# Kernel tuning notes

Measured on AMD Instinct MI355X. Metric: run time of the kernel, lower is better.

Reference implementation:

```python
import jax, jax.numpy as jnp
import numpy as np


def setup_inputs() -> dict:
    key = jax.random.key(0)
    ks = jax.random.split(key, 8)
    B, W, H, C = 4, 64, 64, 256
    C2 = C // 2
    s = 0.05
    x = jax.random.normal(ks[0], (B, W, H, C), dtype=jnp.float32)
    Wq = jax.random.normal(ks[1], (C, C2), dtype=jnp.float32) * s
    bq = jax.random.normal(ks[2], (C2,), dtype=jnp.float32) * s
    Wk = jax.random.normal(ks[3], (C, C2), dtype=jnp.float32) * s
    bk = jax.random.normal(ks[4], (C2,), dtype=jnp.float32) * s
    Wv = jax.random.normal(ks[5], (C, C), dtype=jnp.float32) * s
    bv = jax.random.normal(ks[6], (C,), dtype=jnp.float32) * s
    # gamma is initialized to 0 in the original; use a nonzero value so the
    # attention branch actually contributes (math is identical).
    gamma = jnp.array([0.5], dtype=jnp.float32)
    return {"x": x, "Wq": Wq, "bq": bq, "Wk": Wk, "bk": bk, "Wv": Wv, "bv": bv, "gamma": gamma}


def reference(x, Wq, bq, Wk, bk, Wv, bv, gamma):
    B, W, H, C = x.shape
    N = W * H
    # 1x1 convs == per-pixel linear projections
    q = jnp.einsum('bwhc,cd->bwhd', x, Wq) + bq   # [B,W,H,C/2]
    k = jnp.einsum('bwhc,cd->bwhd', x, Wk) + bk   # [B,W,H,C/2]
    v = jnp.einsum('bwhc,cd->bwhd', x, Wv) + bv   # [B,W,H,C]
    # Faithful to original: raw row-major reshape (B,W,H,Cq) -> (B,Cq,N)
    # (this mixes spatial and channel axes, exactly as the TF code does)
    pq = q.reshape(B, -1, N)                      # [B,C/2,N]
    pk = k.reshape(B, -1, N)                      # [B,C/2,N]
    pv = v.reshape(B, -1, N)                      # [B,C,N]
    energy = jnp.einsum('bcn,bcm->bnm', pq, pk)   # [B,N,N] (pq transposed)
    attention = jax.nn.softmax(energy, axis=-1)   # [B,N,N]
    out = jnp.einsum('bcm,bnm->bcn', pv, attention)  # pv @ attention^T
    out = out.reshape(B, W, H, C)
    return gamma * out + x
```

## Files before the change

kernel.cpp:

```cpp
#include <hip/hip_runtime.h>
#include <hip/hip_bf16.h>
#include <stdint.h>


typedef __attribute__((ext_vector_type(8)))  short short8;
typedef __attribute__((ext_vector_type(4)))  float f32x4;
typedef __attribute__((ext_vector_type(16))) float f32x16;
typedef __attribute__((ext_vector_type(4)))  unsigned short u16x4;

#define MFMA16 __builtin_amdgcn_mfma_f32_16x16x32_bf16
#define MFMA32 __builtin_amdgcn_mfma_f32_32x32x16_bf16

__device__ __forceinline__ unsigned short f2bf(float f) {
    union { float f; uint32_t u; } v; v.f = f;
    return (unsigned short)((v.u + 0x8000u) >> 16);
}
__device__ __forceinline__ float bf2f(unsigned short h) {
    union { uint32_t u; float f; } v; v.u = ((uint32_t)h) << 16;
    return v.f;
}
__device__ __forceinline__ uint32_t pkbf(float a, float b) {
    union { __hip_bfloat162 h; uint32_t u; } v;
    v.h = __float22bfloat162_rn(float2{a, b});
    return v.u;
}

__global__ void prep_w(const float* __restrict__ Wq, const float* __restrict__ bq,
                       const float* __restrict__ Wk, const float* __restrict__ bk,
                       const float* __restrict__ Wv, const float* __restrict__ bv,
                       unsigned short* __restrict__ Wt, float* __restrict__ bias) {
    int g = blockIdx.x * 256 + threadIdx.x;
    int c = g & 255, d = g >> 8;
    float val;
    if (d < 128)      val = Wq[c * 128 + d];
    else if (d < 256) val = Wk[c * 128 + (d - 128)];
    else              val = Wv[c * 256 + (d - 256)];
    Wt[d * 256 + c] = f2bf(val);
    if (g < 512) {
        float bb;
        if (g < 128)      bb = bq[g];
        else if (g < 256) bb = bk[g - 128];
        else              bb = bv[g - 256];
        bias[g] = bb;
    }
}

__global__ __launch_bounds__(256) void proj(
        const float* __restrict__ x, const unsigned short* __restrict__ Wt,
        const float* __restrict__ bias,
        unsigned short* __restrict__ Qrm, unsigned short* __restrict__ Kp,
        unsigned short* __restrict__ Vp) {
    __shared__ unsigned short T[128 * 136];
    int bid = blockIdx.x;
    int tid = threadIdx.x;
    int wave = tid >> 6, lane = tid & 63;
    int l16 = lane & 15, quad = lane >> 4;

    int kind, b, a, vh = 0;
    if (bid < 256) { kind = bid >> 7; int s = bid & 127; b = s >> 5; a = s & 31; }
    else           { kind = 2; int s = bid - 256; vh = s >> 7; b = (s >> 5) & 3; a = s & 31; }

    short8 af[2][8];
    #pragma unroll
    for (int g = 0; g < 2; ++g) {
        int p_local = wave * 32 + g * 16 + l16;
        int pix = (kind == 2) ? (b * 4096 + a * 128 + p_local)
                              : (b * 4096 + a + 32 * p_local);
        const float* xr = x + (size_t)pix * 256;
        #pragma unroll
        for (int kk = 0; kk < 8; ++kk) {
            f32x4 u0 = *(const f32x4*)(xr + kk * 32 + quad * 8);
            f32x4 u1 = *(const f32x4*)(xr + kk * 32 + quad * 8 + 4);
            union { short8 s; uint32_t u[4]; } h;
            h.u[0] = pkbf(u0[0], u0[1]); h.u[1] = pkbf(u0[2], u0[3]);
            h.u[2] = pkbf(u1[0], u1[1]); h.u[3] = pkbf(u1[2], u1[3]);
            af[g][kk] = h.s;
        }
    }

    if (kind < 2) {
        int dbase = kind * 128;
        #pragma unroll 1
        for (int dt = 0; dt < 8; ++dt) {
            int d = dbase + dt * 16 + l16;
            float bval = bias[d];
            f32x4 acc0 = {0.f,0.f,0.f,0.f}, acc1 = {0.f,0.f,0.f,0.f};
            #pragma unroll
            for (int kk = 0; kk < 8; ++kk) {
                short8 wrow = *(const short8*)(Wt + d * 256 + kk * 32 + quad * 8);
                acc0 = MFMA16(af[0][kk], wrow, acc0, 0, 0, 0);
                acc1 = MFMA16(af[1][kk], wrow, acc1, 0, 0, 0);
            }
            #pragma unroll
            for (int g = 0; g < 2; ++g) {
                f32x4 acc = g ? acc1 : acc0;
                union { u16x4 v; uint32_t u[2]; } pk;
                pk.u[0] = pkbf(acc[0] + bval, acc[1] + bval);
                pk.u[1] = pkbf(acc[2] + bval, acc[3] + bval);
                *(u16x4*)(T + (dt * 16 + l16) * 136 + wave * 32 + g * 16 + quad * 4) = pk.v;
            }
        }
        __syncthreads();
        if (kind == 0) {
            unsigned short* ob = Qrm + (b << 19) + a * 128 * 128;
            #pragma unroll
            for (int it = 0; it < 8; ++it) {
                int ci = it * 256 + tid;
                int row = ci >> 4, cj = ci & 15;
                *(short8*)(ob + row * 128 + cj * 8) = *(const short8*)(T + row * 136 + cj * 8);
            }
        } else {
            unsigned short* kb = Kp + (b << 19);
            #pragma unroll
            for (int it = 0; it < 8; ++it) {
                int ci = it * 256 + tid;
                int row = ci >> 4, cj = ci & 15;
                *(short8*)(kb + (cj >> 1) * 65536 + (a * 128 + row) * 16 + (cj & 1) * 8)
                    = *(const short8*)(T + row * 136 + cj * 8);
            }
        }
    } else {
        #pragma unroll 1
        for (int dt = 0; dt < 8; ++dt) {
            int d = 256 + vh * 128 + dt * 16 + l16;
            f32x4 acc0 = {0.f,0.f,0.f,0.f}, acc1 = {0.f,0.f,0.f,0.f};
            #pragma unroll
            for (int kk = 0; kk < 8; ++kk) {
                short8 wrow = *(const short8*)(Wt + d * 256 + kk * 32 + quad * 8);
                acc0 = MFMA16(wrow, af[0][kk], acc0, 0, 0, 0);
                acc1 = MFMA16(wrow, af[1][kk], acc1, 0, 0, 0);
            }
            int dvl = dt * 16 + quad * 4;
            f32x4 bv4 = *(const f32x4*)(bias + 256 + vh * 128 + dvl);
            #pragma unroll
            for (int g = 0; g < 2; ++g) {
                f32x4 acc = g ? acc1 : acc0;
                union { u16x4 v; uint32_t u[2]; } pk;
                pk.u[0] = pkbf(acc[0] + bv4[0], acc[1] + bv4[1]);
                pk.u[1] = pkbf(acc[2] + bv4[2], acc[3] + bv4[3]);
                int p_local = wave * 32 + g * 16 + l16;
                *(u16x4*)(T + p_local * 136 + dvl) = pk.v;
            }
        }
        __syncthreads();
        unsigned short* vb = Vp + (b << 20);
        #pragma unroll
        for (int it = 0; it < 8; ++it) {
            int cid = it * 256 + tid;
            int c_local = cid >> 8, w = cid & 255;
            int p_local = c_local * 16 + (w >> 4);
            int chunk = (w >> 4) * 16 + vh * 8 + ((w & 15) >> 1);
            *(short8*)(vb + chunk * 4096 + (a * 8 + c_local) * 16 + (w & 1) * 8)
                = *(const short8*)(T + p_local * 136 + (w & 15) * 8);
        }
    }
}

__global__ __launch_bounds__(256, 2) void attn(
        const unsigned short* __restrict__ Qrm, const unsigned short* __restrict__ Kp,
        const unsigned short* __restrict__ Vp, unsigned short* __restrict__ Opart,
        float* __restrict__ Lpart) {
    __shared__ unsigned short Ps[2 * 64 * 72];

    int bid = blockIdx.x;
    int comb = bid & 7, qt = bid >> 3;
    int b = comb >> 1, ks = comb & 1;
    int tid = threadIdx.x, wave = tid >> 6, lane = tid & 63;
    int l32 = lane & 31, half = lane >> 5;
    int mt = wave & 1, nt = wave >> 1;

    const unsigned short* Qb = Qrm + (b << 19);
    const unsigned short* Kb = Kp + (b << 19);
    const unsigned short* Vb = Vp + (b << 20);

    int q0 = qt * 64;

    short8 qf[8];
    {
        const unsigned short* qrow = Qb + (q0 + nt * 32 + l32) * 128 + half * 8;
        #pragma unroll
        for (int kk = 0; kk < 8; ++kk) qf[kk] = *(const short8*)(qrow + kk * 16);
    }

    f32x16 O[2][2];
    #pragma unroll
    for (int i = 0; i < 2; ++i)
        #pragma unroll
        for (int j = 0; j < 2; ++j)
            #pragma unroll
            for (int r = 0; r < 16; ++r) O[i][j][r] = 0.f;
    float l_run = 0.f;

    const int m_base = ks * 2048;
    const int chunk_base = ks * 128;

    int krow = (m_base + mt * 32 + l32) * 16 + half * 8;
    short8 kf[8];
    #pragma unroll
    for (int kk = 0; kk < 8; ++kk)
        kf[kk] = *(const short8*)(Kb + kk * 65536 + krow);
    short8 vfrag[2][4];
    #pragma unroll
    for (int c2 = 0; c2 < 2; ++c2)
        #pragma unroll
        for (int k2 = 0; k2 < 4; ++k2)
            vfrag[c2][k2] = *(const short8*)(Vb + (chunk_base + k2) * 4096
                              + ((wave * 2 + c2) * 32 + l32) * 16 + half * 8);

    #pragma unroll 1
    for (int kt = 0; kt < 32; ++kt) {
        unsigned short* Pb = Ps + (kt & 1) * (64 * 72);

        f32x16 S;
        #pragma unroll
        for (int r = 0; r < 16; ++r) S[r] = 0.f;
        #pragma unroll
        for (int kk = 0; kk < 8; ++kk) S = MFMA32(kf[kk], qf[kk], S, 0, 0, 0);

        #pragma unroll
        for (int g = 0; g < 4; ++g) {
            float p0 = __expf(S[g * 4 + 0]), p1 = __expf(S[g * 4 + 1]);
            float p2 = __expf(S[g * 4 + 2]), p3 = __expf(S[g * 4 + 3]);
            l_run += (p0 + p1) + (p2 + p3);
            union { u16x4 v; uint32_t u[2]; } pk;
            pk.u[0] = pkbf(p0, p1); pk.u[1] = pkbf(p2, p3);
            *(u16x4*)(Pb + (nt * 32 + l32) * 72 + mt * 32 + g * 8 + half * 4) = pk.v;
        }

        __syncthreads();

        if (kt < 31) {
            int kr1 = (m_base + (kt + 1) * 64 + mt * 32 + l32) * 16 + half * 8;
            #pragma unroll
            for (int kk = 0; kk < 8; ++kk)
                kf[kk] = *(const short8*)(Kb + kk * 65536 + kr1);
        }

        #pragma unroll
        for (int k2 = 0; k2 < 4; ++k2) {
            short8 pa0 = *(const short8*)(Pb + (l32) * 72 + k2 * 16 + half * 8);
            short8 pa1 = *(const short8*)(Pb + (32 + l32) * 72 + k2 * 16 + half * 8);
            O[0][0] = MFMA32(pa0, vfrag[0][k2], O[0][0], 0, 0, 0);
            O[0][1] = MFMA32(pa0, vfrag[1][k2], O[0][1], 0, 0, 0);
            O[1][0] = MFMA32(pa1, vfrag[0][k2], O[1][0], 0, 0, 0);
            O[1][1] = MFMA32(pa1, vfrag[1][k2], O[1][1], 0, 0, 0);
        }

        if (kt < 31) {
            int ch1 = chunk_base + (kt + 1) * 4;
            #pragma unroll
            for (int c2 = 0; c2 < 2; ++c2)
                #pragma unroll
                for (int k2 = 0; k2 < 4; ++k2)
                    vfrag[c2][k2] = *(const short8*)(Vb + (ch1 + k2) * 4096
                                      + ((wave * 2 + c2) * 32 + l32) * 16 + half * 8);
        }
    }

    l_run += __shfl_xor(l_run, 32);
    unsigned short* Op = Opart + ((size_t)(ks * 4 + b) << 20);
    #pragma unroll
    for (int q2 = 0; q2 < 2; ++q2)
        #pragma unroll
        for (int c2 = 0; c2 < 2; ++c2) {
            int c = (wave * 2 + c2) * 32 + l32;
            #pragma unroll
            for (int r = 0; r < 16; ++r) {
                int n = q0 + q2 * 32 + (r & 3) + 8 * (r >> 2) + 4 * half;
                Op[(size_t)n * 256 + c] = f2bf(O[q2][c2][r]);
            }
        }
    if (half == 0) {
        int n = q0 + nt * 32 + l32;
        Lpart[((ks * 2 + mt) * 4 + b) * 4096 + n] = l_run;
    }
}

__global__ __launch_bounds__(256) void merge_out(
        const unsigned short* __restrict__ Opart, const float* __restrict__ Lpart,
        const float* __restrict__ x, const float* __restrict__ gamma,
        float* __restrict__ out) {
    __shared__ float tile[64 * 257];
    __shared__ float wsm[64];
    int b  = blockIdx.x >> 6;
    int n0 = (blockIdx.x & 63) << 6;
    int tid = threadIdx.x;
    float g = gamma[0];
    if (tid < 64) {
        int n = n0 + tid;
        float L = 0.f;
        #pragma unroll
        for (int s = 0; s < 4; ++s) L += Lpart[(s * 4 + b) * 4096 + n];
        wsm[tid] = g / L;
    }
    __syncthreads();
    int nl1 = tid >> 5, cb1 = (tid & 31) * 8;
    const unsigned short* Op0 = Opart + ((size_t)(0 * 4 + b) << 20);
    const unsigned short* Op1 = Opart + ((size_t)(1 * 4 + b) << 20);
    #pragma unroll
    for (int i = 0; i < 8; ++i) {
        int nl = i * 8 + nl1;
        size_t off = (size_t)(n0 + nl) * 256 + cb1;
        short8 o0 = *(const short8*)(Op0 + off);
        short8 o1 = *(const short8*)(Op1 + off);
        float w = wsm[nl];
        float* tr = tile + nl * 257 + cb1;
        #pragma unroll
        for (int e = 0; e < 8; ++e)
            tr[e] = (bf2f((unsigned short)o0[e]) + bf2f((unsigned short)o1[e])) * w;
    }
    __syncthreads();
    int cg = tid >> 4, nq = (tid & 15) * 4;
    #pragma unroll
    for (int it = 0; it < 16; ++it) {
        int c = it * 16 + cg;
        size_t idx = ((size_t)b << 20) + (size_t)c * 4096 + n0 + nq;
        f32x4 xv = *(const f32x4*)(x + idx);
        f32x4 ov;
        #pragma unroll
        for (int e = 0; e < 4; ++e) ov[e] = tile[(nq + e) * 257 + c] + xv[e];
        *(f32x4*)(out + idx) = ov;
    }
}

extern "C" void kernel_launch(void* const* d_in, const int* in_sizes, int n_in,
                              void* d_out, int out_size, void* d_ws, size_t ws_size,
                              hipStream_t stream) {
    const float* x     = (const float*)d_in[0];
    const float* Wq    = (const float*)d_in[1];
    const float* bq    = (const float*)d_in[2];
    const float* Wk    = (const float*)d_in[3];
    const float* bk    = (const float*)d_in[4];
    const float* Wv    = (const float*)d_in[5];
    const float* bv    = (const float*)d_in[6];
    const float* gamma = (const float*)d_in[7];
    float* out = (float*)d_out;

    if (ws_size < 34080768u) return;

    char* ws = (char*)d_ws;
    unsigned short* Wt    = (unsigned short*)(ws);
    float*          bias  = (float*)        (ws +   262144);
    unsigned short* Qrm   = (unsigned short*)(ws +   264192);
    unsigned short* Kp    = (unsigned short*)(ws +  4458496);
    unsigned short* Vp    = (unsigned short*)(ws +  8652800);
    unsigned short* Opart = (unsigned short*)(ws + 17041408);
    float*          Lpart = (float*)        (ws + 33818624);

    prep_w   <<<512, 256, 0, stream>>>(Wq, bq, Wk, bk, Wv, bv, Wt, bias);
    proj     <<<512, 256, 0, stream>>>(x, Wt, bias, Qrm, Kp, Vp);
    attn     <<<512, 256, 0, stream>>>(Qrm, Kp, Vp, Opart, Lpart);
    merge_out<<<256, 256, 0, stream>>>(Opart, Lpart, x, gamma, out);
}
```

Measured before the change: 175.4 us.

## Fuse merge into attention kernel and drop key-split partials

Restructures the attention kernel so each block handles 32 query rows over the full key range instead of 64 rows over half the keys. Softmax normalization, gamma scaling and the residual add now happen in the attention epilogue via shared memory, which removes the bf16 partial-output buffers and the separate merge kernel. The goal is to cut global traffic for the partials and one kernel launch. In exchange, each block does half the query rows, so K and V fragments are loaded twice as often per query, and more vfrag registers may lower occupancy.

```diff
diff --git a/kernel.cpp b/kernel.cpp
--- a/kernel.cpp
+++ b/kernel.cpp
@@ -14,10 +14,6 @@
 __device__ __forceinline__ unsigned short f2bf(float f) {
     union { float f; uint32_t u; } v; v.f = f;
     return (unsigned short)((v.u + 0x8000u) >> 16);
-}
-__device__ __forceinline__ float bf2f(unsigned short h) {
-    union { uint32_t u; float f; } v; v.u = ((uint32_t)h) << 16;
-    return v.f;
 }
 __device__ __forceinline__ uint32_t pkbf(float a, float b) {
     union { __hip_bfloat162 h; uint32_t u; } v;
@@ -158,58 +154,58 @@
 
 __global__ __launch_bounds__(256, 2) void attn(
         const unsigned short* __restrict__ Qrm, const unsigned short* __restrict__ Kp,
-        const unsigned short* __restrict__ Vp, unsigned short* __restrict__ Opart,
-        float* __restrict__ Lpart) {
-    __shared__ unsigned short Ps[2 * 64 * 72];
+        const unsigned short* __restrict__ Vp, const float* __restrict__ x,
+        const float* __restrict__ gamma, float* __restrict__ out) {
+    __shared__ __align__(16) char smem[256 * 36 * 4];
+    __shared__ float Ls[4][32];
+    __shared__ float lwv[32];
+    unsigned short* Ps = (unsigned short*)smem;
+    float* Os = (float*)smem;
 
     int bid = blockIdx.x;
-    int comb = bid & 7, qt = bid >> 3;
-    int b = comb >> 1, ks = comb & 1;
+    int b = bid & 3, qt = bid >> 2;
     int tid = threadIdx.x, wave = tid >> 6, lane = tid & 63;
     int l32 = lane & 31, half = lane >> 5;
-    int mt = wave & 1, nt = wave >> 1;
 
     const unsigned short* Qb = Qrm + (b << 19);
     const unsigned short* Kb = Kp + (b << 19);
     const unsigned short* Vb = Vp + (b << 20);
 
-    int q0 = qt * 64;
+    int n0 = qt * 32;
+    float gm = gamma[0];
 
     short8 qf[8];
     {
-        const unsigned short* qrow = Qb + (q0 + nt * 32 + l32) * 128 + half * 8;
+        const unsigned short* qrow = Qb + (n0 + l32) * 128 + half * 8;
         #pragma unroll
         for (int kk = 0; kk < 8; ++kk) qf[kk] = *(const short8*)(qrow + kk * 16);
     }
 
-    f32x16 O[2][2];
-    #pragma unroll
-    for (int i = 0; i < 2; ++i)
-        #pragma unroll
-        for (int j = 0; j < 2; ++j)
-            #pragma unroll
-            for (int r = 0; r < 16; ++r) O[i][j][r] = 0.f;
+    f32x16 O[2];
+    #pragma unroll
+    for (int j = 0; j < 2; ++j)
+        #pragma unroll
+        for (int r = 0; r < 16; ++r) O[j][r] = 0.f;
     float l_run = 0.f;
 
-    const int m_base = ks * 2048;
-    const int chunk_base = ks * 128;
-
-    int krow = (m_base + mt * 32 + l32) * 16 + half * 8;
     short8 kf[8];
-    #pragma unroll
-    for (int kk = 0; kk < 8; ++kk)
-        kf[kk] = *(const short8*)(Kb + kk * 65536 + krow);
-    short8 vfrag[2][4];
+    {
+        int m0 = (wave * 32 + l32) * 16 + half * 8;
+        #pragma unroll
+        for (int kk = 0; kk < 8; ++kk)
+            kf[kk] = *(const short8*)(Kb + kk * 65536 + m0);
+    }
+    short8 vfrag[2][8];
     #pragma unroll
     for (int c2 = 0; c2 < 2; ++c2)
         #pragma unroll
-        for (int k2 = 0; k2 < 4; ++k2)
-            vfrag[c2][k2] = *(const short8*)(Vb + (chunk_base + k2) * 4096
+        for (int k2 = 0; k2 < 8; ++k2)
+            vfrag[c2][k2] = *(const short8*)(Vb + k2 * 4096
                               + ((wave * 2 + c2) * 32 + l32) * 16 + half * 8);
 
     #pragma unroll 1
     for (int kt = 0; kt < 32; ++kt) {
-        unsigned short* Pb = Ps + (kt & 1) * (64 * 72);
+        unsigned short* Pb = Ps + (kt & 1) * (32 * 136);
 
         f32x16 S;
         #pragma unroll
@@ -224,102 +220,68 @@
             l_run += (p0 + p1) + (p2 + p3);
             union { u16x4 v; uint32_t u[2]; } pk;
             pk.u[0] = pkbf(p0, p1); pk.u[1] = pkbf(p2, p3);
-            *(u16x4*)(Pb + (nt * 32 + l32) * 72 + mt * 32 + g * 8 + half * 4) = pk.v;
+            *(u16x4*)(Pb + l32 * 136 + wave * 32 + g * 8 + half * 4) = pk.v;
         }
 
         __syncthreads();
 
         if (kt < 31) {
-            int kr1 = (m_base + (kt + 1) * 64 + mt * 32 + l32) * 16 + half * 8;
+            int m1 = ((kt + 1) * 128 + wave * 32 + l32) * 16 + half * 8;
             #pragma unroll
             for (int kk = 0; kk < 8; ++kk)
-                kf[kk] = *(const short8*)(Kb + kk * 65536 + kr1);
-        }
-
-        #pragma unroll
-        for (int k2 = 0; k2 < 4; ++k2) {
-            short8 pa0 = *(const short8*)(Pb + (l32) * 72 + k2 * 16 + half * 8);
-            short8 pa1 = *(const short8*)(Pb + (32 + l32) * 72 + k2 * 16 + half * 8);
-            O[0][0] = MFMA32(pa0, vfrag[0][k2], O[0][0], 0, 0, 0);
-            O[0][1] = MFMA32(pa0, vfrag[1][k2], O[0][1], 0, 0, 0);
-            O[1][0] = MFMA32(pa1, vfrag[0][k2], O[1][0], 0, 0, 0);
-            O[1][1] = MFMA32(pa1, vfrag[1][k2], O[1][1], 0, 0, 0);
+                kf[kk] = *(const short8*)(Kb + kk * 65536 + m1);
+        }
+
+        #pragma unroll
+        for (int k2 = 0; k2 < 8; ++k2) {
+            short8 pa = *(const short8*)(Pb + l32 * 136 + k2 * 16 + half * 8);
+            O[0] = MFMA32(pa, vfrag[0][k2], O[0], 0, 0, 0);
+            O[1] = MFMA32(pa, vfrag[1][k2], O[1], 0, 0, 0);
         }
 
         if (kt < 31) {
-            int ch1 = chunk_base + (kt + 1) * 4;
+            int ch1 = (kt + 1) * 8;
             #pragma unroll
             for (int c2 = 0; c2 < 2; ++c2)
                 #pragma unroll
-                for (int k2 = 0; k2 < 4; ++k2)
+                for (int k2 = 0; k2 < 8; ++k2)
                     vfrag[c2][k2] = *(const short8*)(Vb + (ch1 + k2) * 4096
                                       + ((wave * 2 + c2) * 32 + l32) * 16 + half * 8);
         }
     }
 
     l_run += __shfl_xor(l_run, 32);
-    unsigned short* Op = Opart + ((size_t)(ks * 4 + b) << 20);
-    #pragma unroll
-    for (int q2 = 0; q2 < 2; ++q2)
-        #pragma unroll
-        for (int c2 = 0; c2 < 2; ++c2) {
-            int c = (wave * 2 + c2) * 32 + l32;
-            #pragma unroll
-            for (int r = 0; r < 16; ++r) {
-                int n = q0 + q2 * 32 + (r & 3) + 8 * (r >> 2) + 4 * half;
-                Op[(size_t)n * 256 + c] = f2bf(O[q2][c2][r]);
-            }
-        }
-    if (half == 0) {
-        int n = q0 + nt * 32 + l32;
-        Lpart[((ks * 2 + mt) * 4 + b) * 4096 + n] = l_run;
-    }
-}
-
-__global__ __launch_bounds__(256) void merge_out(
-        const unsigned short* __restrict__ Opart, const float* __restrict__ Lpart,
-        const float* __restrict__ x, const float* __restrict__ gamma,
-        float* __restrict__ out) {
-    __shared__ float tile[64 * 257];
-    __shared__ float wsm[64];
-    int b  = blockIdx.x >> 6;
-    int n0 = (blockIdx.x & 63) << 6;
-    int tid = threadIdx.x;
-    float g = gamma[0];
-    if (tid < 64) {
-        int n = n0 + tid;
-        float L = 0.f;
-        #pragma unroll
-        for (int s = 0; s < 4; ++s) L += Lpart[(s * 4 + b) * 4096 + n];
-        wsm[tid] = g / L;
-    }
+    if (half == 0) Ls[wave][l32] = l_run;
     __syncthreads();
-    int nl1 = tid >> 5, cb1 = (tid & 31) * 8;
-    const unsigned short* Op0 = Opart + ((size_t)(0 * 4 + b) << 20);
-    const unsigned short* Op1 = Opart + ((size_t)(1 * 4 + b) << 20);
-    #pragma unroll
-    for (int i = 0; i < 8; ++i) {
-        int nl = i * 8 + nl1;
-        size_t off = (size_t)(n0 + nl) * 256 + cb1;
-        short8 o0 = *(const short8*)(Op0 + off);
-        short8 o1 = *(const short8*)(Op1 + off);
-        float w = wsm[nl];
-        float* tr = tile + nl * 257 + cb1;
-        #pragma unroll
-        for (int e = 0; e < 8; ++e)
-            tr[e] = (bf2f((unsigned short)o0[e]) + bf2f((unsigned short)o1[e])) * w;
-    }
+    if (tid < 32)
+        lwv[tid] = gm / (Ls[0][tid] + Ls[1][tid] + Ls[2][tid] + Ls[3][tid]);
     __syncthreads();
-    int cg = tid >> 4, nq = (tid & 15) * 4;
-    #pragma unroll
-    for (int it = 0; it < 16; ++it) {
-        int c = it * 16 + cg;
-        size_t idx = ((size_t)b << 20) + (size_t)c * 4096 + n0 + nq;
+
+    #pragma unroll
+    for (int c2 = 0; c2 < 2; ++c2) {
+        int c = (wave * 2 + c2) * 32 + l32;
+        #pragma unroll
+        for (int g = 0; g < 4; ++g) {
+            f32x4 gv = *(const f32x4*)(lwv + g * 8 + half * 4);
+            f32x4 ov;
+            #pragma unroll
+            for (int i = 0; i < 4; ++i) ov[i] = O[c2][g * 4 + i] * gv[i];
+            *(f32x4*)(Os + c * 36 + g * 8 + half * 4) = ov;
+        }
+    }
+    __syncthreads();
+
+    int n4 = tid & 7, cg = tid >> 3;
+    #pragma unroll
+    for (int it = 0; it < 8; ++it) {
+        int c = it * 32 + cg;
+        f32x4 ov = *(const f32x4*)(Os + c * 36 + n4 * 4);
+        size_t idx = ((size_t)b << 20) + (size_t)c * 4096 + n0 + n4 * 4;
         f32x4 xv = *(const f32x4*)(x + idx);
-        f32x4 ov;
-        #pragma unroll
-        for (int e = 0; e < 4; ++e) ov[e] = tile[(nq + e) * 257 + c] + xv[e];
-        *(f32x4*)(out + idx) = ov;
+        f32x4 rv;
+        #pragma unroll
+        for (int e = 0; e < 4; ++e) rv[e] = ov[e] + xv[e];
+        *(f32x4*)(out + idx) = rv;
     }
 }
 
@@ -336,7 +298,7 @@
     const float* gamma = (const float*)d_in[7];
     float* out = (float*)d_out;
 
-    if (ws_size < 34080768u) return;
+    if (ws_size < 17041408u) return;
 
     char* ws = (char*)d_ws;
     unsigned short* Wt    = (unsigned short*)(ws);
@@ -344,11 +306,8 @@
     unsigned short* Qrm   = (unsigned short*)(ws +   264192);
     unsigned short* Kp    = (unsigned short*)(ws +  4458496);
     unsigned short* Vp    = (unsigned short*)(ws +  8652800);
-    unsigned short* Opart = (unsigned short*)(ws + 17041408);
-    float*          Lpart = (float*)        (ws + 33818624);
-
-    prep_w   <<<512, 256, 0, stream>>>(Wq, bq, Wk, bk, Wv, bv, Wt, bias);
-    proj     <<<512, 256, 0, stream>>>(x, Wt, bias, Qrm, Kp, Vp);
-    attn     <<<512, 256, 0, stream>>>(Qrm, Kp, Vp, Opart, Lpart);
-    merge_out<<<256, 256, 0, stream>>>(Opart, Lpart, x, gamma, out);
-}
+
+    prep_w<<<512, 256, 0, stream>>>(Wq, bq, Wk, bk, Wv, bv, Wt, bias);
+    proj  <<<512, 256, 0, stream>>>(x, Wt, bias, Qrm, Kp, Vp);
+    attn  <<<512, 256, 0, stream>>>(Qrm, Kp, Vp, x, gamma, out);
+}
```

Result: slower. 180.8 us (+3.1%).

## Fuse all four phases into one cooperative kernel with grid-wide syncs

Applied to the files above, without the earlier changes.

Turns the prep, projection, attention and merge kernels into device phases and runs them inside a single cooperative kernel of 512 blocks, separated by grid.sync(), with shared memory reused across phases. The merge phase is re-tiled to 32 rows per block so it also uses 512 blocks. This aims to remove the launch gaps and tail idle time between the four launches. In exchange it adds grid-barrier cost, forces one launch-bounds and shared-memory size on all phases, and falls back to separate launches if the cooperative launch fails.

```diff
diff --git a/kernel.cpp b/kernel.cpp
--- a/kernel.cpp
+++ b/kernel.cpp
@@ -1,6 +1,9 @@
 #include <hip/hip_runtime.h>
 #include <hip/hip_bf16.h>
+#include <hip/hip_cooperative_groups.h>
 #include <stdint.h>
+
+namespace cg = cooperative_groups;
 
 
 typedef __attribute__((ext_vector_type(8)))  short short8;
@@ -11,6 +14,8 @@
 #define MFMA16 __builtin_amdgcn_mfma_f32_16x16x32_bf16
 #define MFMA32 __builtin_amdgcn_mfma_f32_32x32x16_bf16
 
+#define SMEM_BYTES 34816
+
 __device__ __forceinline__ unsigned short f2bf(float f) {
     union { float f; uint32_t u; } v; v.f = f;
     return (unsigned short)((v.u + 0x8000u) >> 16);
@@ -25,11 +30,13 @@
     return v.u;
 }
 
-__global__ void prep_w(const float* __restrict__ Wq, const float* __restrict__ bq,
-                       const float* __restrict__ Wk, const float* __restrict__ bk,
-                       const float* __restrict__ Wv, const float* __restrict__ bv,
-                       unsigned short* __restrict__ Wt, float* __restrict__ bias) {
-    int g = blockIdx.x * 256 + threadIdx.x;
+__device__ __forceinline__ void phase_prep(
+        int bid, int tid,
+        const float* __restrict__ Wq, const float* __restrict__ bq,
+        const float* __restrict__ Wk, const float* __restrict__ bk,
+        const float* __restrict__ Wv, const float* __restrict__ bv,
+        unsigned short* __restrict__ Wt, float* __restrict__ bias) {
+    int g = bid * 256 + tid;
     int c = g & 255, d = g >> 8;
     float val;
     if (d < 128)      val = Wq[c * 128 + d];
@@ -45,14 +52,13 @@
     }
 }
 
-__global__ __launch_bounds__(256) void proj(
+__device__ __forceinline__ void phase_proj(
+        char* smem, int bid, int tid,
         const float* __restrict__ x, const unsigned short* __restrict__ Wt,
         const float* __restrict__ bias,
         unsigned short* __restrict__ Qrm, unsigned short* __restrict__ Kp,
         unsigned short* __restrict__ Vp) {
-    __shared__ unsigned short T[128 * 136];
-    int bid = blockIdx.x;
-    int tid = threadIdx.x;
+    unsigned short* T = (unsigned short*)smem;
     int wave = tid >> 6, lane = tid & 63;
     int l16 = lane & 15, quad = lane >> 4;
 
@@ -156,16 +162,16 @@
     }
 }
 
-__global__ __launch_bounds__(256, 2) void attn(
+__device__ __forceinline__ void phase_attn(
+        char* smem, int bid, int tid,
         const unsigned short* __restrict__ Qrm, const unsigned short* __restrict__ Kp,
         const unsigned short* __restrict__ Vp, unsigned short* __restrict__ Opart,
         float* __restrict__ Lpart) {
-    __shared__ unsigned short Ps[2 * 64 * 72];
-
-    int bid = blockIdx.x;
+    unsigned short* Ps = (unsigned short*)smem;
+
     int comb = bid & 7, qt = bid >> 3;
     int b = comb >> 1, ks = comb & 1;
-    int tid = threadIdx.x, wave = tid >> 6, lane = tid & 63;
+    int wave = tid >> 6, lane = tid & 63;
     int l32 = lane & 31, half = lane >> 5;
     int mt = wave & 1, nt = wave >> 1;
 
@@ -204,7 +210,7 @@
     for (int c2 = 0; c2 < 2; ++c2)
         #pragma unroll
         for (int k2 = 0; k2 < 4; ++k2)
-            vfrag[c2][k2] = *(const short8*)(Vb + (chunk_base + k2) * 4096
+            vfrag[c2][k2] = *(const short8*)(Vp + (b << 20) + (chunk_base + k2) * 4096
                               + ((wave * 2 + c2) * 32 + l32) * 16 + half * 8);
 
     #pragma unroll 1
@@ -276,17 +282,17 @@
     }
 }
 
-__global__ __launch_bounds__(256) void merge_out(
+__device__ __forceinline__ void phase_merge(
+        char* smem, int bid, int tid,
         const unsigned short* __restrict__ Opart, const float* __restrict__ Lpart,
         const float* __restrict__ x, const float* __restrict__ gamma,
         float* __restrict__ out) {
-    __shared__ float tile[64 * 257];
-    __shared__ float wsm[64];
-    int b  = blockIdx.x >> 6;
-    int n0 = (blockIdx.x & 63) << 6;
-    int tid = threadIdx.x;
+    float* tile = (float*)smem;
+    float* wsm  = (float*)smem + 32 * 257;
+    int b  = bid >> 7;
+    int n0 = (bid & 127) << 5;
     float g = gamma[0];
-    if (tid < 64) {
+    if (tid < 32) {
         int n = n0 + tid;
         float L = 0.f;
         #pragma unroll
@@ -295,10 +301,10 @@
     }
     __syncthreads();
     int nl1 = tid >> 5, cb1 = (tid & 31) * 8;
-    const unsigned short* Op0 = Opart + ((size_t)(0 * 4 + b) << 20);
-    const unsigned short* Op1 = Opart + ((size_t)(1 * 4 + b) << 20);
-    #pragma unroll
-    for (int i = 0; i < 8; ++i) {
+    const unsigned short* Op0 = Opart + ((size_t)b << 20);
+    const unsigned short* Op1 = Opart + ((size_t)(4 + b) << 20);
+    #pragma unroll
+    for (int i = 0; i < 4; ++i) {
         int nl = i * 8 + nl1;
         size_t off = (size_t)(n0 + nl) * 256 + cb1;
         short8 o0 = *(const short8*)(Op0 + off);
@@ -310,10 +316,10 @@
             tr[e] = (bf2f((unsigned short)o0[e]) + bf2f((unsigned short)o1[e])) * w;
     }
     __syncthreads();
-    int cg = tid >> 4, nq = (tid & 15) * 4;
-    #pragma unroll
-    for (int it = 0; it < 16; ++it) {
-        int c = it * 16 + cg;
+    int cg2 = tid >> 3, nq = (tid & 7) * 4;
+    #pragma unroll
+    for (int it = 0; it < 8; ++it) {
+        int c = it * 32 + cg2;
         size_t idx = ((size_t)b << 20) + (size_t)c * 4096 + n0 + nq;
         f32x4 xv = *(const f32x4*)(x + idx);
         f32x4 ov;
@@ -321,6 +327,49 @@
         for (int e = 0; e < 4; ++e) ov[e] = tile[(nq + e) * 257 + c] + xv[e];
         *(f32x4*)(out + idx) = ov;
     }
+}
+
+__global__ void __launch_bounds__(256, 2) fused_all(
+        const float* x, const float* Wq, const float* bq, const float* Wk,
+        const float* bk, const float* Wv, const float* bv, const float* gamma,
+        float* out, unsigned short* Wt, float* bias, unsigned short* Qrm,
+        unsigned short* Kp, unsigned short* Vp, unsigned short* Opart,
+        float* Lpart) {
+    __shared__ __align__(16) char smem[SMEM_BYTES];
+    cg::grid_group grid = cg::this_grid();
+    int bid = blockIdx.x, tid = threadIdx.x;
+
+    phase_prep(bid, tid, Wq, bq, Wk, bk, Wv, bv, Wt, bias);
+    grid.sync();
+    phase_proj(smem, bid, tid, x, Wt, bias, Qrm, Kp, Vp);
+    grid.sync();
+    phase_attn(smem, bid, tid, Qrm, Kp, Vp, Opart, Lpart);
+    grid.sync();
+    phase_merge(smem, bid, tid, Opart, Lpart, x, gamma, out);
+}
+
+__global__ void prep_w_k(const float* Wq, const float* bq, const float* Wk,
+                         const float* bk, const float* Wv, const float* bv,
+                         unsigned short* Wt, float* bias) {
+    phase_prep(blockIdx.x, threadIdx.x, Wq, bq, Wk, bk, Wv, bv, Wt, bias);
+}
+__global__ __launch_bounds__(256) void proj_k(
+        const float* x, const unsigned short* Wt, const float* bias,
+        unsigned short* Qrm, unsigned short* Kp, unsigned short* Vp) {
+    __shared__ __align__(16) char smem[SMEM_BYTES];
+    phase_proj(smem, blockIdx.x, threadIdx.x, x, Wt, bias, Qrm, Kp, Vp);
+}
+__global__ __launch_bounds__(256, 2) void attn_k(
+        const unsigned short* Qrm, const unsigned short* Kp,
+        const unsigned short* Vp, unsigned short* Opart, float* Lpart) {
+    __shared__ __align__(16) char smem[18432];
+    phase_attn(smem, blockIdx.x, threadIdx.x, Qrm, Kp, Vp, Opart, Lpart);
+}
+__global__ __launch_bounds__(256) void merge_k(
+        const unsigned short* Opart, const float* Lpart, const float* x,
+        const float* gamma, float* out) {
+    __shared__ __align__(16) char smem[33024];
+    phase_merge(smem, blockIdx.x, threadIdx.x, Opart, Lpart, x, gamma, out);
 }
 
 extern "C" void kernel_launch(void* const* d_in, const int* in_sizes, int n_in,
@@ -347,8 +396,17 @@
     unsigned short* Opart = (unsigned short*)(ws + 17041408);
     float*          Lpart = (float*)        (ws + 33818624);
 
-    prep_w   <<<512, 256, 0, stream>>>(Wq, bq, Wk, bk, Wv, bv, Wt, bias);
-    proj     <<<512, 256, 0, stream>>>(x, Wt, bias, Qrm, Kp, Vp);
-    attn     <<<512, 256, 0, stream>>>(Qrm, Kp, Vp, Opart, Lpart);
-    merge_out<<<256, 256, 0, stream>>>(Opart, Lpart, x, gamma, out);
-}
+    void* args[] = { (void*)&x, (void*)&Wq, (void*)&bq, (void*)&Wk, (void*)&bk,
+                     (void*)&Wv, (void*)&bv, (void*)&gamma, (void*)&out,
+                     (void*)&Wt, (void*)&bias, (void*)&Qrm, (void*)&Kp,
+                     (void*)&Vp, (void*)&Opart, (void*)&Lpart };
+    hipError_t err = hipLaunchCooperativeKernel((const void*)fused_all,
+                                                dim3(512), dim3(256),
+                                                args, 0, stream);
+    if (err != hipSuccess) {
+        prep_w_k<<<512, 256, 0, stream>>>(Wq, bq, Wk, bk, Wv, bv, Wt, bias);
+        proj_k  <<<512, 256, 0, stream>>>(x, Wt, bias, Qrm, Kp, Vp);
+        attn_k  <<<512, 256, 0, stream>>>(Qrm, Kp, Vp, Opart, Lpart);
+        merge_k <<<512, 256, 0, stream>>>(Opart, Lpart, x, gamma, out);
+    }
+}
```

Measured after the change: 365.9 us. +108.6%, slower.

## Software-pipeline QK^T and softmax one tile ahead of PV in attention loop

Applied to the files above, without the earlier changes.

Restructures the main attention loop so the S=K·Q MFMA, exp, and P store for tile kt+1 run before the PV MFMAs of tile kt. K fragments are prefetched two tiles ahead. This lets the exp/VALU work overlap with the matrix-core work across the barrier and hides K load latency better. The cost is higher register pressure from holding extra prefetched K fragments, plus a prologue that duplicates the first tile's work.

```diff
diff --git a/kernel.cpp b/kernel.cpp
--- a/kernel.cpp
+++ b/kernel.cpp
@@ -193,12 +193,12 @@
 
     const int m_base = ks * 2048;
     const int chunk_base = ks * 128;
-
-    int krow = (m_base + mt * 32 + l32) * 16 + half * 8;
+    const int kbase = (m_base + mt * 32 + l32) * 16 + half * 8;
+
     short8 kf[8];
     #pragma unroll
     for (int kk = 0; kk < 8; ++kk)
-        kf[kk] = *(const short8*)(Kb + kk * 65536 + krow);
+        kf[kk] = *(const short8*)(Kb + kk * 65536 + kbase);
     short8 vfrag[2][4];
     #pragma unroll
     for (int c2 = 0; c2 < 2; ++c2)
@@ -206,17 +206,12 @@
         for (int k2 = 0; k2 < 4; ++k2)
             vfrag[c2][k2] = *(const short8*)(Vb + (chunk_base + k2) * 4096
                               + ((wave * 2 + c2) * 32 + l32) * 16 + half * 8);
-
-    #pragma unroll 1
-    for (int kt = 0; kt < 32; ++kt) {
-        unsigned short* Pb = Ps + (kt & 1) * (64 * 72);
-
+    {
         f32x16 S;
         #pragma unroll
         for (int r = 0; r < 16; ++r) S[r] = 0.f;
         #pragma unroll
         for (int kk = 0; kk < 8; ++kk) S = MFMA32(kf[kk], qf[kk], S, 0, 0, 0);
-
         #pragma unroll
         for (int g = 0; g < 4; ++g) {
             float p0 = __expf(S[g * 4 + 0]), p1 = __expf(S[g * 4 + 1]);
@@ -224,18 +219,42 @@
             l_run += (p0 + p1) + (p2 + p3);
             union { u16x4 v; uint32_t u[2]; } pk;
             pk.u[0] = pkbf(p0, p1); pk.u[1] = pkbf(p2, p3);
-            *(u16x4*)(Pb + (nt * 32 + l32) * 72 + mt * 32 + g * 8 + half * 4) = pk.v;
-        }
-
+            *(u16x4*)(Ps + (nt * 32 + l32) * 72 + mt * 32 + g * 8 + half * 4) = pk.v;
+        }
+        #pragma unroll
+        for (int kk = 0; kk < 8; ++kk)
+            kf[kk] = *(const short8*)(Kb + kk * 65536 + 64 * 16 + kbase);
+    }
+
+    #pragma unroll 1
+    for (int kt = 0; kt < 32; ++kt) {
         __syncthreads();
 
         if (kt < 31) {
-            int kr1 = (m_base + (kt + 1) * 64 + mt * 32 + l32) * 16 + half * 8;
-            #pragma unroll
-            for (int kk = 0; kk < 8; ++kk)
-                kf[kk] = *(const short8*)(Kb + kk * 65536 + kr1);
-        }
-
+            f32x16 S;
+            #pragma unroll
+            for (int r = 0; r < 16; ++r) S[r] = 0.f;
+            #pragma unroll
+            for (int kk = 0; kk < 8; ++kk) S = MFMA32(kf[kk], qf[kk], S, 0, 0, 0);
+            if (kt < 30) {
+                int kr = (kt + 2) * 64 * 16 + kbase;
+                #pragma unroll
+                for (int kk = 0; kk < 8; ++kk)
+                    kf[kk] = *(const short8*)(Kb + kk * 65536 + kr);
+            }
+            unsigned short* Pn = Ps + ((kt + 1) & 1) * (64 * 72);
+            #pragma unroll
+            for (int g = 0; g < 4; ++g) {
+                float p0 = __expf(S[g * 4 + 0]), p1 = __expf(S[g * 4 + 1]);
+                float p2 = __expf(S[g * 4 + 2]), p3 = __expf(S[g * 4 + 3]);
+                l_run += (p0 + p1) + (p2 + p3);
+                union { u16x4 v; uint32_t u[2]; } pk;
+                pk.u[0] = pkbf(p0, p1); pk.u[1] = pkbf(p2, p3);
+                *(u16x4*)(Pn + (nt * 32 + l32) * 72 + mt * 32 + g * 8 + half * 4) = pk.v;
+            }
+        }
+
+        unsigned short* Pb = Ps + (kt & 1) * (64 * 72);
         #pragma unroll
         for (int k2 = 0; k2 < 4; ++k2) {
             short8 pa0 = *(const short8*)(Pb + (l32) * 72 + k2 * 16 + half * 8);
@@ -295,8 +314,8 @@
     }
     __syncthreads();
     int nl1 = tid >> 5, cb1 = (tid & 31) * 8;
-    const unsigned short* Op0 = Opart + ((size_t)(0 * 4 + b) << 20);
-    const unsigned short* Op1 = Opart + ((size_t)(1 * 4 + b) << 20);
+    const unsigned short* Op0 = Opart + ((size_t)b << 20);
+    const unsigned short* Op1 = Opart + ((size_t)(4 + b) << 20);
     #pragma unroll
     for (int i = 0; i < 8; ++i) {
         int nl = i * 8 + nl1;
```

Measured after the change: 172.5 us. About the same (-1.6%).
